# Optimization experiments

Hardware: AMD Instinct MI355X
Metric: run time of the kernel (lower is better)

## Reference

```python
import jax, jax.numpy as jnp
import numpy as np


def setup_inputs() -> dict:
    key = jax.random.key(0)
    kq, kk, kv = jax.random.split(key, 3)
    B, H, T, D = 1, 16, 4096, 64
    Q = jax.random.normal(kq, (B, H, T, D), dtype=jnp.float32)
    K = jax.random.normal(kk, (B, H, T, D), dtype=jnp.float32)
    V = jax.random.normal(kv, (B, H, T, D), dtype=jnp.float32)
    return {"Q": Q, "K": K, "V": V}


def reference(Q, K, V):
    B, H, T, D = Q.shape
    # ALiBi slopes: m_h = 2^(-8*h/H), h = 1..H (deterministic buffer)
    slopes = jnp.exp2(-8.0 * jnp.arange(1, H + 1, dtype=jnp.float32) / H)
    pos = jnp.arange(T, dtype=jnp.float32)
    dist = jnp.abs(pos[None, :] - pos[:, None])          # (T, T)
    bias = slopes[:, None, None] * dist                   # (H, T, T)
    scale = jnp.sqrt(jnp.asarray(D, dtype=Q.dtype))
    scores = jnp.einsum('bhtd,bhsd->bhts', Q, K) / scale - bias[None]
    attn = jax.nn.softmax(scores, axis=-1)
    return jnp.einsum('bhts,bhsd->bhtd', attn, V)
```

## Files before the change

kernel.cpp:

```cpp
#include <hip/hip_runtime.h>
#include <hip/hip_bf16.h>
#include <stdint.h>

typedef float f4    __attribute__((ext_vector_type(4)));
typedef float f32x4 __attribute__((ext_vector_type(4)));
typedef short s16x8 __attribute__((ext_vector_type(8)));
typedef short s16x4 __attribute__((ext_vector_type(4)));
typedef unsigned short u16;

#define T_LEN 4096
#define NHEAD 16
#define DHEAD 64
#define KVBLK 64
#define NT    (T_LEN / KVBLK)

#if __has_builtin(__builtin_amdgcn_exp2f)
#define EXP2(x) __builtin_amdgcn_exp2f(x)
#else
#define EXP2(x) exp2f(x)
#endif

#define SLOT_F 8320
#define CONV_BYTES ((size_t)16777216)
#define SLOTS_BAL  1152
#define BAL_BYTES  (CONV_BYTES + (size_t)SLOTS_BAL * SLOT_F * 4u)

__device__ __constant__ int NCARR[8] = {2,2,3,5,6,6,6,6};
__device__ __constant__ int SBARR[8] = {1088,1024,928,768,576,384,192,0};

__device__ __forceinline__ uint32_t pk2(float a, float b){
  uint32_t ua = __builtin_bit_cast(uint32_t, a) + 0x8000u;
  uint32_t ub = __builtin_bit_cast(uint32_t, b) + 0x8000u;
  return __builtin_amdgcn_perm(ub, ua, 0x07060302u);
}
__device__ __forceinline__ int swk(int r){ return (r ^ (r >> 3)) & 7; }
__device__ __forceinline__ int sw(int r){ return swk(r) << 3; }

__global__ __launch_bounds__(256)
void cvt_kv(const float* __restrict__ K, const float* __restrict__ V,
            u16* __restrict__ Kb, u16* __restrict__ VT){
  __shared__ u16 tile[64][66];
  if (blockIdx.x < 2048){
    const size_t i = ((size_t)blockIdx.x * 256 + threadIdx.x) * 8;
    f4 a = *(const f4*)(K + i);
    f4 b = *(const f4*)(K + i + 4);
    union { uint32_t w[4]; s16x8 v; } u;
    u.w[0] = pk2(a[0], a[1]); u.w[1] = pk2(a[2], a[3]);
    u.w[2] = pk2(b[0], b[1]); u.w[3] = pk2(b[2], b[3]);
    *(s16x8*)(Kb + i) = u.v;
  } else {
    const int vb = blockIdx.x - 2048;
    const int h  = vb >> 6;
    const int kt = vb & 63;
    const int t  = threadIdx.x;
    const float* Vh = V + ((size_t)h * T_LEN + kt * 64) * DHEAD;

    const int r = t >> 2, c = (t & 3) * 16;
    f4 x0 = *(const f4*)(Vh + r*64 + c);
    f4 x1 = *(const f4*)(Vh + r*64 + c + 4);
    f4 x2 = *(const f4*)(Vh + r*64 + c + 8);
    f4 x3 = *(const f4*)(Vh + r*64 + c + 12);
    uint32_t* tp = (uint32_t*)&tile[r][c];
    tp[0] = pk2(x0[0],x0[1]); tp[1] = pk2(x0[2],x0[3]);
    tp[2] = pk2(x1[0],x1[1]); tp[3] = pk2(x1[2],x1[3]);
    tp[4] = pk2(x2[0],x2[1]); tp[5] = pk2(x2[2],x2[3]);
    tp[6] = pk2(x3[0],x3[1]); tp[7] = pk2(x3[2],x3[3]);
    __syncthreads();

    const int d = t >> 2, ks = (t & 3) * 16;
    u16* op = VT + ((size_t)h * DHEAD + d) * T_LEN + kt * 64 + ks;
    union { uint32_t w[4]; s16x8 v; } o0, o1;
#pragma unroll
    for (int q = 0; q < 4; ++q)
      o0.w[q] = (uint32_t)tile[ks + 2*q][d]     | ((uint32_t)tile[ks + 2*q + 1][d] << 16);
#pragma unroll
    for (int q = 0; q < 4; ++q)
      o1.w[q] = (uint32_t)tile[ks + 8 + 2*q][d] | ((uint32_t)tile[ks + 9 + 2*q][d] << 16);
    *(s16x8*)(op)     = o0.v;
    *(s16x8*)(op + 8) = o1.v;
  }
}

__global__ __launch_bounds__(256, 2)
void alibi_attn8(const float* __restrict__ Qg,
                 const u16* __restrict__ Kb,
                 const u16* __restrict__ VTb,
                 float* __restrict__ Og,
                 float* __restrict__ part)
{
  __shared__ u16 kbuf[2][KVBLK * DHEAD];
  __shared__ u16 vbuf[2][DHEAD * KVBLK];

  int h, qt, c, n, sb;
  {
    int r = blockIdx.x;
    if (r < 768){
      h = 15 - r / 192; r %= 192; n = 6; qt = r / 6; c = r % 6; sb = (15 - h) * 192;
    } else if ((r -= 768) < 160){
      h = 11; n = 5; qt = r / 5; c = r % 5; sb = 768;
    } else if ((r -= 160) < 96){
      h = 10; n = 3; qt = r / 3; c = r % 3; sb = 928;
    } else if ((r -= 96) < 64){
      h = 9; n = 2; qt = r >> 1; c = r & 1; sb = 1024;
    } else if ((r -= 64) < 64){
      h = 8; n = 2; qt = r >> 1; c = r & 1; sb = 1088;
    } else {
      r -= 64; h = r >> 5; qt = r & 31; n = 1; c = 0; sb = 0;
    }
  }

  const int tid  = threadIdx.x;
  const int wv   = tid >> 6;
  const int lane = tid & 63;
  const int lg   = lane >> 4;
  const int ln   = lane & 15;

  const int q0   = qt * 128;
  const int qr0  = q0 + wv * 32 + ln;
  const float slope = exp2f(-0.5f * (float)(h + 1));
  const float cs = 0.125f * 1.44269504089f;
  const float bs = slope * 1.44269504089f;
  const size_t headoff = (size_t)h * T_LEN * DHEAD;

  const int Di = (int)(36.0f / bs);
  int lo = (q0 - Di) >> 6;           if (lo < 0) lo = 0;
  int hi = (q0 + 127 + Di) >> 6;     if (hi > NT - 1) hi = NT - 1;
  const int len = hi - lo + 1;
  const int start = lo + (c * len) / n;
  const int end   = lo + ((c + 1) * len) / n;

  s16x8 qf[2][2];
#pragma unroll
  for (int rg = 0; rg < 2; ++rg){
    const float* qp = Qg + headoff + (size_t)(qr0 + rg*16) * DHEAD + lg * 8;
    f4 x = *(const f4*)qp;        f4 y = *(const f4*)(qp + 4);
    f4 z = *(const f4*)(qp + 32); f4 v = *(const f4*)(qp + 36);
    union { uint32_t w_[4]; s16x8 v_; } u0, u1;
    u0.w_[0] = pk2(x[0]*cs, x[1]*cs); u0.w_[1] = pk2(x[2]*cs, x[3]*cs);
    u0.w_[2] = pk2(y[0]*cs, y[1]*cs); u0.w_[3] = pk2(y[2]*cs, y[3]*cs);
    u1.w_[0] = pk2(z[0]*cs, z[1]*cs); u1.w_[1] = pk2(z[2]*cs, z[3]*cs);
    u1.w_[2] = pk2(v[0]*cs, v[1]*cs); u1.w_[3] = pk2(v[2]*cs, v[3]*cs);
    qf[rg][0] = u0.v_; qf[rg][1] = u1.v_;
  }

  f32x4 acc[2][4];
#pragma unroll
  for (int rg = 0; rg < 2; ++rg)
#pragma unroll
    for (int dt = 0; dt < 4; ++dt) acc[rg][dt] = (f32x4)(0.0f);
  float lsum[2] = {0.0f, 0.0f};
  const float b0 = (float)qr0 - (float)(lg * 4);

  int koffs[4][2];
#pragma unroll
  for (int kt = 0; kt < 4; ++kt){
    const int key = kt*16 + ln, sz = sw(key);
    koffs[kt][0] = (((key*64      + lg*8) ^ sz)) * 2;
    koffs[kt][1] = (((key*64 + 32 + lg*8) ^ sz)) * 2;
  }
  int voffs[4][4];
#pragma unroll
  for (int dt = 0; dt < 4; ++dt){
    const int d = dt*16 + ln, sz = sw(d);
#pragma unroll
    for (int kt = 0; kt < 4; ++kt)
      voffs[dt][kt] = (((d*64 + kt*16 + lg*4) ^ sz)) * 2;
  }

  const u16* Kh = Kb  + headoff;
  const u16* Vh = VTb + headoff;
  const int sA = wv * 128 + lane;
  const int sB = sA + 64;
  const int keyA = sA >> 3, gA = (sA & 7) ^ swk(keyA);
  const int keyB = sB >> 3, gB = (sB & 7) ^ swk(keyB);
  const int kidxA = keyA * 64 + gA * 8;
  const int kidxB = keyB * 64 + gB * 8;
  const int vidxA = keyA * T_LEN + gA * 8;
  const int vidxB = keyB * T_LEN + gB * 8;
  const int dstA = sA * 16, dstB = sB * 16;

  s16x8 rkA, rkB, rvA, rvB;
  auto ldregs = [&](int t){
    const u16* kp = Kh + (size_t)t * (KVBLK * DHEAD);
    const u16* vp = Vh + (size_t)t * KVBLK;
    rkA = *(const s16x8*)(kp + kidxA);  rkB = *(const s16x8*)(kp + kidxB);
    rvA = *(const s16x8*)(vp + vidxA);  rvB = *(const s16x8*)(vp + vidxB);
  };
  auto wrregs = [&](u16* kb_, u16* vb_){
    *(s16x8*)((char*)kb_ + dstA) = rkA;  *(s16x8*)((char*)kb_ + dstB) = rkB;
    *(s16x8*)((char*)vb_ + dstA) = rvA;  *(s16x8*)((char*)vb_ + dstB) = rvB;
  };

  auto compute = [&](const u16* kb_, const u16* vb_, int kv){
    f32x4 S[2][4];
    __builtin_amdgcn_s_setprio(1);
#pragma unroll
    for (int kt = 0; kt < 4; ++kt){
      s16x8 k0 = *(const s16x8*)((const char*)kb_ + koffs[kt][0]);
      s16x8 k1 = *(const s16x8*)((const char*)kb_ + koffs[kt][1]);
      f32x4 c0 = (f32x4)(0.0f), c1 = (f32x4)(0.0f);
      c0 = __builtin_amdgcn_mfma_f32_16x16x32_bf16(k0, qf[0][0], c0, 0, 0, 0);
      c0 = __builtin_amdgcn_mfma_f32_16x16x32_bf16(k1, qf[0][1], c0, 0, 0, 0);
      c1 = __builtin_amdgcn_mfma_f32_16x16x32_bf16(k0, qf[1][0], c1, 0, 0, 0);
      c1 = __builtin_amdgcn_mfma_f32_16x16x32_bf16(k1, qf[1][1], c1, 0, 0, 0);
      S[0][kt] = c0; S[1][kt] = c1;
    }
    __builtin_amdgcn_s_setprio(0);

    s16x4 pb[2][4];
#pragma unroll
    for (int rg = 0; rg < 2; ++rg){
      const float bi = b0 + (float)(rg * 16) - (float)(kv * KVBLK);
#pragma unroll
      for (int kt = 0; kt < 4; ++kt)
#pragma unroll
        for (int r = 0; r < 4; ++r)
          S[rg][kt][r] = EXP2(fmaf(-bs, fabsf(bi - (float)(kt*16 + r)), S[rg][kt][r]));

      lsum[rg] += (((S[rg][0][0]+S[rg][0][1]) + (S[rg][0][2]+S[rg][0][3]))
                +  ((S[rg][1][0]+S[rg][1][1]) + (S[rg][1][2]+S[rg][1][3])))
                + (((S[rg][2][0]+S[rg][2][1]) + (S[rg][2][2]+S[rg][2][3]))
                +  ((S[rg][3][0]+S[rg][3][1]) + (S[rg][3][2]+S[rg][3][3])));

#pragma unroll
      for (int kt = 0; kt < 4; ++kt){
        union { uint32_t w_[2]; s16x4 v_; } u;
        u.w_[0] = pk2(S[rg][kt][0], S[rg][kt][1]);
        u.w_[1] = pk2(S[rg][kt][2], S[rg][kt][3]);
        pb[rg][kt] = u.v_;
      }
    }

    __builtin_amdgcn_s_setprio(1);
#pragma unroll
    for (int dt = 0; dt < 4; ++dt){
#pragma unroll
      for (int kt = 0; kt < 4; ++kt){
        const s16x4 vf = *(const s16x4*)((const char*)vb_ + voffs[dt][kt]);
        acc[0][dt] = __builtin_amdgcn_mfma_f32_16x16x16bf16_1k(vf, pb[0][kt], acc[0][dt], 0, 0, 0);
        acc[1][dt] = __builtin_amdgcn_mfma_f32_16x16x16bf16_1k(vf, pb[1][kt], acc[1][dt], 0, 0, 0);
      }
    }
    __builtin_amdgcn_s_setprio(0);
  };

  {
    ldregs(start);
    wrregs(kbuf[0], vbuf[0]);
    __syncthreads();

    const int hi_i = end - 1;
    int t = start;
#pragma unroll 1
    while (t + 1 < hi_i){
      ldregs(t + 1);
      compute(kbuf[0], vbuf[0], t);
      wrregs(kbuf[1], vbuf[1]);
      __syncthreads();
      ldregs(t + 2);
      compute(kbuf[1], vbuf[1], t + 1);
      wrregs(kbuf[0], vbuf[0]);
      __syncthreads();
      t += 2;
    }
    if (t < hi_i){
      ldregs(t + 1);
      compute(kbuf[0], vbuf[0], t);
      wrregs(kbuf[1], vbuf[1]);
      __syncthreads();
      compute(kbuf[1], vbuf[1], t + 1);
    } else {
      compute(kbuf[0], vbuf[0], t);
    }
  }

#pragma unroll
  for (int rg = 0; rg < 2; ++rg){
    lsum[rg] += __shfl_xor(lsum[rg], 16, 64);
    lsum[rg] += __shfl_xor(lsum[rg], 32, 64);
  }

  if (n == 1){
#pragma unroll
    for (int rg = 0; rg < 2; ++rg){
      const float inv = 1.0f / lsum[rg];
      float* op = Og + headoff + (size_t)(qr0 + rg*16) * DHEAD + lg * 4;
#pragma unroll
      for (int dt = 0; dt < 4; ++dt){
        f4 o;
        o[0] = acc[rg][dt][0] * inv; o[1] = acc[rg][dt][1] * inv;
        o[2] = acc[rg][dt][2] * inv; o[3] = acc[rg][dt][3] * inv;
        *(f4*)(op + dt*16) = o;
      }
    }
  } else {
    float* slot = part + (size_t)(sb + qt * n + c) * SLOT_F;
#pragma unroll
    for (int rg = 0; rg < 2; ++rg){
      const int row = wv * 32 + rg * 16 + ln;
      float* op = slot + row * 64 + lg * 4;
#pragma unroll
      for (int dt = 0; dt < 4; ++dt)
        *(f4*)(op + dt*16) = acc[rg][dt];
      if (lg == 0) slot[8192 + row] = lsum[rg];
    }
  }
}

__global__ __launch_bounds__(256)
void combine_k(const float* __restrict__ part, float* __restrict__ Og){
  const int h  = 8 + (blockIdx.x >> 5);
  const int qt = blockIdx.x & 31;
  const int n  = NCARR[h - 8];
  const int sb = SBARR[h - 8] + qt * n;

  const int t   = threadIdx.x;
  const int row = t >> 1;
  const int seg = (t & 1) * 32;

  f4 a[8];
#pragma unroll
  for (int i = 0; i < 8; ++i) a[i] = (f4)(0.0f);
  float l = 0.0f;
#pragma unroll 1
  for (int c = 0; c < n; ++c){
    const float* sp = part + (size_t)(sb + c) * SLOT_F;
    const float* rp = sp + row * 64 + seg;
#pragma unroll
    for (int i = 0; i < 8; ++i) a[i] += *(const f4*)(rp + i*4);
    l += sp[8192 + row];
  }
  const float inv = 1.0f / l;
  float* op = Og + (((size_t)h * T_LEN + qt * 128 + row) * DHEAD) + seg;
#pragma unroll
  for (int i = 0; i < 8; ++i){
    f4 o;
    o[0] = a[i][0]*inv; o[1] = a[i][1]*inv; o[2] = a[i][2]*inv; o[3] = a[i][3]*inv;
    *(f4*)(op + i*4) = o;
  }
}

__global__ __launch_bounds__(256, 4)
void alibi_attn4(const float* __restrict__ Qg,
                 const u16* __restrict__ Kb,
                 const u16* __restrict__ VTb,
                 float* __restrict__ Og)
{
  __shared__ u16 kbuf[2][KVBLK * DHEAD];
  __shared__ u16 vbuf[2][DHEAD * KVBLK];

  const int bid = blockIdx.x;
  const int fid = (bid & 7) * 128 + (bid >> 3);
  const int h  = fid & 15;
  const int qt = fid >> 4;

  const int tid  = threadIdx.x;
  const int wv   = tid >> 6;
  const int lane = tid & 63;
  const int lg   = lane >> 4;
  const int ln   = lane & 15;

  const int q0   = qt * 64;
  const int qrow = q0 + wv * 16 + ln;
  const float slope = exp2f(-0.5f * (float)(h + 1));
  const float cs = 0.125f * 1.44269504089f;
  const float bs = slope * 1.44269504089f;
  const size_t headoff = (size_t)h * T_LEN * DHEAD;

  const int Di = (int)(36.0f / bs);
  int lo = (q0 - Di) >> 6;           if (lo < 0) lo = 0;
  int hi = (q0 + 63 + Di) >> 6;      if (hi > NT - 1) hi = NT - 1;

  s16x8 qf0, qf1;
  {
    const float* qp = Qg + headoff + (size_t)qrow * DHEAD + lg * 8;
    f4 x = *(const f4*)qp;        f4 y = *(const f4*)(qp + 4);
    f4 z = *(const f4*)(qp + 32); f4 v = *(const f4*)(qp + 36);
    union { uint32_t w_[4]; s16x8 v_; } u0, u1;
    u0.w_[0] = pk2(x[0]*cs, x[1]*cs); u0.w_[1] = pk2(x[2]*cs, x[3]*cs);
    u0.w_[2] = pk2(y[0]*cs, y[1]*cs); u0.w_[3] = pk2(y[2]*cs, y[3]*cs);
    u1.w_[0] = pk2(z[0]*cs, z[1]*cs); u1.w_[1] = pk2(z[2]*cs, z[3]*cs);
    u1.w_[2] = pk2(v[0]*cs, v[1]*cs); u1.w_[3] = pk2(v[2]*cs, v[3]*cs);
    qf0 = u0.v_; qf1 = u1.v_;
  }

  f32x4 acc[4];
#pragma unroll
  for (int dt = 0; dt < 4; ++dt) acc[dt] = (f32x4)(0.0f);
  float lsum = 0.0f;
  const float base0 = (float)qrow - (float)(lg * 4);

  int koffs[4][2];
#pragma unroll
  for (int kt = 0; kt < 4; ++kt){
    const int key = kt*16 + ln, sz = sw(key);
    koffs[kt][0] = (((key*64      + lg*8) ^ sz)) * 2;
    koffs[kt][1] = (((key*64 + 32 + lg*8) ^ sz)) * 2;
  }
  int voffs[4][4];
#pragma unroll
  for (int dt = 0; dt < 4; ++dt){
    const int d = dt*16 + ln, sz = sw(d);
#pragma unroll
    for (int kt = 0; kt < 4; ++kt)
      voffs[dt][kt] = (((d*64 + kt*16 + lg*4) ^ sz)) * 2;
  }

  const u16* Kh = Kb  + headoff;
  const u16* Vh = VTb + headoff;
  const int sA = wv * 128 + lane;
  const int sB = sA + 64;
  const int keyA = sA >> 3, gA = (sA & 7) ^ swk(keyA);
  const int keyB = sB >> 3, gB = (sB & 7) ^ swk(keyB);
  const int kidxA = keyA * 64 + gA * 8;
  const int kidxB = keyB * 64 + gB * 8;
  const int vidxA = keyA * T_LEN + gA * 8;
  const int vidxB = keyB * T_LEN + gB * 8;
  const int dstA = sA * 16, dstB = sB * 16;

  s16x8 rkA, rkB, rvA, rvB;
  auto ldregs = [&](int t){
    const u16* kp = Kh + (size_t)t * (KVBLK * DHEAD);
    const u16* vp = Vh + (size_t)t * KVBLK;
    rkA = *(const s16x8*)(kp + kidxA);  rkB = *(const s16x8*)(kp + kidxB);
    rvA = *(const s16x8*)(vp + vidxA);  rvB = *(const s16x8*)(vp + vidxB);
  };
  auto wrregs = [&](u16* kb_, u16* vb_){
    *(s16x8*)((char*)kb_ + dstA) = rkA;  *(s16x8*)((char*)kb_ + dstB) = rkB;
    *(s16x8*)((char*)vb_ + dstA) = rvA;  *(s16x8*)((char*)vb_ + dstB) = rvB;
  };

  auto compute = [&](const u16* kb_, const u16* vb_, int kv){
    f32x4 S[4];
    __builtin_amdgcn_s_setprio(1);
#pragma unroll
    for (int kt = 0; kt < 4; ++kt){
      s16x8 k0 = *(const s16x8*)((const char*)kb_ + koffs[kt][0]);
      s16x8 k1 = *(const s16x8*)((const char*)kb_ + koffs[kt][1]);
      f32x4 cc = (f32x4)(0.0f);
      cc = __builtin_amdgcn_mfma_f32_16x16x32_bf16(k0, qf0, cc, 0, 0, 0);
      cc = __builtin_amdgcn_mfma_f32_16x16x32_bf16(k1, qf1, cc, 0, 0, 0);
      S[kt] = cc;
    }
    __builtin_amdgcn_s_setprio(0);

    const float bi = base0 - (float)(kv * KVBLK);
    float p[16];
#pragma unroll
    for (int kt = 0; kt < 4; ++kt)
#pragma unroll
      for (int r = 0; r < 4; ++r)
        p[kt*4 + r] = EXP2(fmaf(-bs, fabsf(bi - (float)(kt*16 + r)), S[kt][r]));

    lsum += (((p[0]+p[1]) + (p[2]+p[3])) + ((p[4]+p[5]) + (p[6]+p[7])))
          + (((p[8]+p[9]) + (p[10]+p[11])) + ((p[12]+p[13]) + (p[14]+p[15])));

    s16x4 pb[4];
#pragma unroll
    for (int kt = 0; kt < 4; ++kt){
      union { uint32_t w_[2]; s16x4 v_; } u;
      u.w_[0] = pk2(p[kt*4+0], p[kt*4+1]);
      u.w_[1] = pk2(p[kt*4+2], p[kt*4+3]);
      pb[kt] = u.v_;
    }

    __builtin_amdgcn_s_setprio(1);
#pragma unroll
    for (int dt = 0; dt < 4; ++dt){
#pragma unroll
      for (int kt = 0; kt < 4; ++kt){
        const s16x4 vf = *(const s16x4*)((const char*)vb_ + voffs[dt][kt]);
        acc[dt] = __builtin_amdgcn_mfma_f32_16x16x16bf16_1k(vf, pb[kt], acc[dt], 0, 0, 0);
      }
    }
    __builtin_amdgcn_s_setprio(0);
  };

  ldregs(lo);
  wrregs(kbuf[0], vbuf[0]);
  __syncthreads();

  int t = lo;
#pragma unroll 1
  while (t + 1 < hi){
    ldregs(t + 1);
    compute(kbuf[0], vbuf[0], t);
    wrregs(kbuf[1], vbuf[1]);
    __syncthreads();
    ldregs(t + 2);
    compute(kbuf[1], vbuf[1], t + 1);
    wrregs(kbuf[0], vbuf[0]);
    __syncthreads();
    t += 2;
  }
  if (t < hi){
    ldregs(t + 1);
    compute(kbuf[0], vbuf[0], t);
    wrregs(kbuf[1], vbuf[1]);
    __syncthreads();
    compute(kbuf[1], vbuf[1], t + 1);
  } else {
    compute(kbuf[0], vbuf[0], t);
  }

  lsum += __shfl_xor(lsum, 16, 64);
  lsum += __shfl_xor(lsum, 32, 64);
  const float inv = 1.0f / lsum;
  float* op = Og + headoff + (size_t)qrow * DHEAD + lg * 4;
#pragma unroll
  for (int dt = 0; dt < 4; ++dt){
    f4 o;
    o[0] = acc[dt][0] * inv; o[1] = acc[dt][1] * inv;
    o[2] = acc[dt][2] * inv; o[3] = acc[dt][3] * inv;
    *(f4*)(op + dt*16) = o;
  }
}

__global__ __launch_bounds__(256, 2)
void alibi_attn_fb(const float* __restrict__ Qg,
                   const float* __restrict__ Kg,
                   const float* __restrict__ Vg,
                   float* __restrict__ Og)
{
  __shared__ u16 kbuf[2][KVBLK * DHEAD];
  __shared__ u16 vbuf[2][DHEAD * KVBLK];

  const int bid = blockIdx.x;
  const int fid = (bid & 7) * 64 + (bid >> 3);
  const int h  = fid >> 5;
  const int qt = fid & 31;

  const int tid  = threadIdx.x;
  const int wave = tid >> 6;
  const int lane = tid & 63;
  const int lg   = lane >> 4;
  const int ln   = lane & 15;

  const int qb = qt * 128 + wave * 32;
  const float slope = exp2f(-0.5f * (float)(h + 1));
  const float cs = 0.125f * 1.44269504089f;
  const float bs = slope * 1.44269504089f;
  const size_t headoff = (size_t)h * T_LEN * DHEAD;

  s16x8 qf[2][2];
#pragma unroll
  for (int rg = 0; rg < 2; ++rg)
#pragma unroll
    for (int dh = 0; dh < 2; ++dh){
      const float* qp = Qg + headoff + (size_t)(qb + rg*16 + ln) * DHEAD + dh*32 + lg*8;
      f4 x = *(const f4*)qp;
      f4 y = *(const f4*)(qp + 4);
      union { uint32_t w[4]; s16x8 v; } u;
      u.w[0] = pk2(x[0]*cs, x[1]*cs);
      u.w[1] = pk2(x[2]*cs, x[3]*cs);
      u.w[2] = pk2(y[0]*cs, y[1]*cs);
      u.w[3] = pk2(y[2]*cs, y[3]*cs);
      qf[rg][dh] = u.v;
    }

  f32x4 acc[2][4];
#pragma unroll
  for (int rg = 0; rg < 2; ++rg)
#pragma unroll
    for (int dt = 0; dt < 4; ++dt) acc[rg][dt] = (f32x4)(0.0f);
  float mreg[2] = {-1e30f, -1e30f};
  float lreg[2] = {0.0f, 0.0f};
  const float qposf[2] = {(float)(qb + ln), (float)(qb + 16 + ln)};
  const float koffb = (float)(lg * 4);

  f4 st4[8];
  const int vk0  = (tid >> 2) * 2;
  const int vseg = (tid & 3) * 16;
  const int krow = (tid - 128) >> 1;
  const int kseg = ((tid - 128) & 1) * 32;
  const float* Vb = Vg + headoff;
  const float* Kb_ = Kg + headoff;

  auto stage_load = [&](int kv){
    const int kb = kv * KVBLK;
    if (tid < 128){
      const float* vp = Vb + (size_t)(kb + vk0) * DHEAD + vseg;
      st4[0] = *(const f4*)(vp);      st4[1] = *(const f4*)(vp + 4);
      st4[2] = *(const f4*)(vp + 8);  st4[3] = *(const f4*)(vp + 12);
      st4[4] = *(const f4*)(vp + 64); st4[5] = *(const f4*)(vp + 68);
      st4[6] = *(const f4*)(vp + 72); st4[7] = *(const f4*)(vp + 76);
    } else {
      const float* kp = Kb_ + (size_t)(kb + krow) * DHEAD + kseg;
#pragma unroll
      for (int j = 0; j < 8; ++j) st4[j] = *(const f4*)(kp + j*4);
    }
  };
  auto stage_store = [&](int b){
    if (tid < 128){
#pragma unroll
      for (int i = 0; i < 16; ++i){
        const int d = vseg + i;
        uint32_t pr = pk2(st4[i>>2][i&3], st4[4 + (i>>2)][i&3]);
        *(uint32_t*)&vbuf[b][(d*64 + vk0) ^ sw(d)] = pr;
      }
    } else {
#pragma unroll
      for (int i = 0; i < 4; ++i){
        union { uint32_t w[4]; s16x8 v; } u;
        u.w[0] = pk2(st4[i*2][0],   st4[i*2][1]);
        u.w[1] = pk2(st4[i*2][2],   st4[i*2][3]);
        u.w[2] = pk2(st4[i*2+1][0], st4[i*2+1][1]);
        u.w[3] = pk2(st4[i*2+1][2], st4[i*2+1][3]);
        *(s16x8*)&kbuf[b][(krow*64 + kseg + i*8) ^ sw(krow)] = u.v;
      }
    }
  };

  stage_load(0);
  stage_store(0);
  __syncthreads();
  int cur = 0;

#pragma unroll 1
  for (int kv = 0; kv < NT; ++kv){
    if (kv + 1 < NT) stage_load(kv + 1);

    const float kbf = (float)(kv * KVBLK);
    const u16* kb_ = kbuf[cur];
    const u16* vb_ = vbuf[cur];

    s16x8 kf[4][2];
#pragma unroll
    for (int kt = 0; kt < 4; ++kt){
      const int key = kt*16 + ln;
      const int sz  = sw(key);
      kf[kt][0] = *(const s16x8*)&kb_[(key*64 +      lg*8) ^ sz];
      kf[kt][1] = *(const s16x8*)&kb_[(key*64 + 32 + lg*8) ^ sz];
    }
    f32x4 S[2][4];
#pragma unroll
    for (int rg = 0; rg < 2; ++rg)
#pragma unroll
      for (int kt = 0; kt < 4; ++kt){
        f32x4 c = (f32x4)(0.0f);
        c = __builtin_amdgcn_mfma_f32_16x16x32_bf16(kf[kt][0], qf[rg][0], c, 0, 0, 0);
        c = __builtin_amdgcn_mfma_f32_16x16x32_bf16(kf[kt][1], qf[rg][1], c, 0, 0, 0);
        S[rg][kt] = c;
      }

    s16x4 pb[2][4];
#pragma unroll
    for (int rg = 0; rg < 2; ++rg){
      const float base = qposf[rg] - kbf - koffb;
#pragma unroll
      for (int kt = 0; kt < 4; ++kt)
#pragma unroll
        for (int r = 0; r < 4; ++r)
          S[rg][kt][r] = fmaf(-bs, fabsf(base - (float)(kt*16 + r)), S[rg][kt][r]);

      float a0 = fmaxf(fmaxf(S[rg][0][0], S[rg][0][1]), fmaxf(S[rg][0][2], S[rg][0][3]));
      float a1 = fmaxf(fmaxf(S[rg][1][0], S[rg][1][1]), fmaxf(S[rg][1][2], S[rg][1][3]));
      float a2 = fmaxf(fmaxf(S[rg][2][0], S[rg][2][1]), fmaxf(S[rg][2][2], S[rg][2][3]));
      float a3 = fmaxf(fmaxf(S[rg][3][0], S[rg][3][1]), fmaxf(S[rg][3][2], S[rg][3][3]));
      float mx = fmaxf(fmaxf(a0, a1), fmaxf(a2, a3));
      mx = fmaxf(mx, __shfl_xor(mx, 16, 64));
      mx = fmaxf(mx, __shfl_xor(mx, 32, 64));

      const float mo = mreg[rg];
      const float mn = fmaxf(mo, mx);
      const float scl = EXP2(mo - mn);
      mreg[rg] = mn;

      float p[16];
#pragma unroll
      for (int kt = 0; kt < 4; ++kt)
#pragma unroll
        for (int r = 0; r < 4; ++r)
          p[kt*4 + r] = EXP2(S[rg][kt][r] - mn);

      float s0 = (p[0]+p[1]) + (p[2]+p[3]);
      float s1 = (p[4]+p[5]) + (p[6]+p[7]);
      float s2 = (p[8]+p[9]) + (p[10]+p[11]);
      float s3 = (p[12]+p[13]) + (p[14]+p[15]);
      float sum = (s0+s1) + (s2+s3);
      sum += __shfl_xor(sum, 16, 64);
      sum += __shfl_xor(sum, 32, 64);
      lreg[rg] = lreg[rg] * scl + sum;

#pragma unroll
      for (int dt = 0; dt < 4; ++dt) acc[rg][dt] *= scl;

#pragma unroll
      for (int kt = 0; kt < 4; ++kt){
        union { uint32_t w[2]; s16x4 v; } u;
        u.w[0] = pk2(p[kt*4+0], p[kt*4+1]);
        u.w[1] = pk2(p[kt*4+2], p[kt*4+3]);
        pb[rg][kt] = u.v;
      }
    }

#pragma unroll
    for (int dt = 0; dt < 4; ++dt){
      const int d  = dt*16 + ln;
      const int sz = sw(d);
#pragma unroll
      for (int kt = 0; kt < 4; ++kt){
        const s16x4 vf = *(const s16x4*)&vb_[(d*64 + kt*16 + lg*4) ^ sz];
        acc[0][dt] = __builtin_amdgcn_mfma_f32_16x16x16bf16_1k(vf, pb[0][kt], acc[0][dt], 0, 0, 0);
        acc[1][dt] = __builtin_amdgcn_mfma_f32_16x16x16bf16_1k(vf, pb[1][kt], acc[1][dt], 0, 0, 0);
      }
    }

    if (kv + 1 < NT){
      stage_store(cur ^ 1);
      __syncthreads();
      cur ^= 1;
    }
  }

#pragma unroll
  for (int rg = 0; rg < 2; ++rg){
    const float inv = 1.0f / lreg[rg];
    float* op = Og + headoff + (size_t)(qb + rg*16 + ln) * DHEAD + lg*4;
#pragma unroll
    for (int dt = 0; dt < 4; ++dt){
      f4 o;
      o[0] = acc[rg][dt][0] * inv;
      o[1] = acc[rg][dt][1] * inv;
      o[2] = acc[rg][dt][2] * inv;
      o[3] = acc[rg][dt][3] * inv;
      *(f4*)(op + dt*16) = o;
    }
  }
}

extern "C" void kernel_launch(void* const* d_in, const int* in_sizes, int n_in,
                              void* d_out, int out_size, void* d_ws, size_t ws_size,
                              hipStream_t stream)
{
  const float* Q = (const float*)d_in[0];
  const float* K = (const float*)d_in[1];
  const float* V = (const float*)d_in[2];
  float* O = (float*)d_out;

  if (ws_size >= BAL_BYTES){
    u16* Kb = (u16*)d_ws;
    u16* VT = Kb + (size_t)NHEAD * T_LEN * DHEAD;
    float* part = (float*)((char*)d_ws + CONV_BYTES);
    hipLaunchKernelGGL(cvt_kv, dim3(3072), dim3(256), 0, stream, K, V, Kb, VT);
    hipLaunchKernelGGL(alibi_attn8, dim3(1408), dim3(256), 0, stream, Q, Kb, VT, O, part);
    hipLaunchKernelGGL(combine_k, dim3(256), dim3(256), 0, stream, part, O);
  } else if (ws_size >= CONV_BYTES){
    u16* Kb = (u16*)d_ws;
    u16* VT = Kb + (size_t)NHEAD * T_LEN * DHEAD;
    hipLaunchKernelGGL(cvt_kv, dim3(3072), dim3(256), 0, stream, K, V, Kb, VT);
    hipLaunchKernelGGL(alibi_attn4, dim3(1024), dim3(256), 0, stream, Q, Kb, VT, O);
  } else {
    hipLaunchKernelGGL(alibi_attn_fb, dim3(512), dim3(256), 0, stream, Q, K, V, O);
  }
}
```

Measured before the change: 86.62 us.

## Triple-buffer K/V tiles in LDS with two-deep register prefetch

Replaces the double-buffered K/V pipeline with a three-slot LDS ring and two sets of staging registers. Global loads are issued two tiles ahead and LDS writes one tile ahead, so only one barrier is needed per tile instead of syncing around each write. This aims to hide global memory latency and reduce barrier stalls. The cost is more LDS per block and more staging registers, which may reduce occupancy or cause spills.

```diff
diff --git a/kernel.cpp b/kernel.cpp
--- a/kernel.cpp
+++ b/kernel.cpp
@@ -82,14 +82,14 @@
 }
 
 __global__ __launch_bounds__(256, 2)
-void alibi_attn8(const float* __restrict__ Qg,
+void alibi_attn9(const float* __restrict__ Qg,
                  const u16* __restrict__ Kb,
                  const u16* __restrict__ VTb,
                  float* __restrict__ Og,
                  float* __restrict__ part)
 {
-  __shared__ u16 kbuf[2][KVBLK * DHEAD];
-  __shared__ u16 vbuf[2][DHEAD * KVBLK];
+  __shared__ u16 kbuf[3][KVBLK * DHEAD];
+  __shared__ u16 vbuf[3][DHEAD * KVBLK];
 
   int h, qt, c, n, sb;
   {
@@ -149,7 +149,7 @@
 #pragma unroll
     for (int dt = 0; dt < 4; ++dt) acc[rg][dt] = (f32x4)(0.0f);
   float lsum[2] = {0.0f, 0.0f};
-  const float b0 = (float)qr0 - (float)(lg * 4);
+  const float b0f = (float)qr0 - (float)(lg * 4);
 
   int koffs[4][2];
 #pragma unroll
@@ -179,16 +179,27 @@
   const int vidxB = keyB * T_LEN + gB * 8;
   const int dstA = sA * 16, dstB = sB * 16;
 
-  s16x8 rkA, rkB, rvA, rvB;
-  auto ldregs = [&](int t){
+  s16x8 Ak0, Ak1, Av0, Av1, Bk0, Bk1, Bv0, Bv1;
+  auto ldset = [&](int t){
     const u16* kp = Kh + (size_t)t * (KVBLK * DHEAD);
     const u16* vp = Vh + (size_t)t * KVBLK;
-    rkA = *(const s16x8*)(kp + kidxA);  rkB = *(const s16x8*)(kp + kidxB);
-    rvA = *(const s16x8*)(vp + vidxA);  rvB = *(const s16x8*)(vp + vidxB);
+    if ((t & 1) == 0){
+      Ak0 = *(const s16x8*)(kp + kidxA);  Ak1 = *(const s16x8*)(kp + kidxB);
+      Av0 = *(const s16x8*)(vp + vidxA);  Av1 = *(const s16x8*)(vp + vidxB);
+    } else {
+      Bk0 = *(const s16x8*)(kp + kidxA);  Bk1 = *(const s16x8*)(kp + kidxB);
+      Bv0 = *(const s16x8*)(vp + vidxA);  Bv1 = *(const s16x8*)(vp + vidxB);
+    }
   };
-  auto wrregs = [&](u16* kb_, u16* vb_){
-    *(s16x8*)((char*)kb_ + dstA) = rkA;  *(s16x8*)((char*)kb_ + dstB) = rkB;
-    *(s16x8*)((char*)vb_ + dstA) = rvA;  *(s16x8*)((char*)vb_ + dstB) = rvB;
+  auto wrset = [&](int t, int b){
+    u16* kb_ = kbuf[b];  u16* vb_ = vbuf[b];
+    if ((t & 1) == 0){
+      *(s16x8*)((char*)kb_ + dstA) = Ak0;  *(s16x8*)((char*)kb_ + dstB) = Ak1;
+      *(s16x8*)((char*)vb_ + dstA) = Av0;  *(s16x8*)((char*)vb_ + dstB) = Av1;
+    } else {
+      *(s16x8*)((char*)kb_ + dstA) = Bk0;  *(s16x8*)((char*)kb_ + dstB) = Bk1;
+      *(s16x8*)((char*)vb_ + dstA) = Bv0;  *(s16x8*)((char*)vb_ + dstB) = Bv1;
+    }
   };
 
   auto compute = [&](const u16* kb_, const u16* vb_, int kv){
@@ -210,7 +221,7 @@
     s16x4 pb[2][4];
 #pragma unroll
     for (int rg = 0; rg < 2; ++rg){
-      const float bi = b0 + (float)(rg * 16) - (float)(kv * KVBLK);
+      const float bi = b0f + (float)(rg * 16) - (float)(kv * KVBLK);
 #pragma unroll
       for (int kt = 0; kt < 4; ++kt)
 #pragma unroll
@@ -245,33 +256,22 @@
   };
 
   {
-    ldregs(start);
-    wrregs(kbuf[0], vbuf[0]);
-    __syncthreads();
-
-    const int hi_i = end - 1;
-    int t = start;
+    ldset(start);
+    if (start + 1 < end) ldset(start + 1);
+    wrset(start, start % 3);
+    asm volatile("s_waitcnt lgkmcnt(0)" ::: "memory");
+    __builtin_amdgcn_s_barrier();
+  }
+
+  int bc = start % 3, bn = (start + 1) % 3, bf_ = (start + 2) % 3;
 #pragma unroll 1
-    while (t + 1 < hi_i){
-      ldregs(t + 1);
-      compute(kbuf[0], vbuf[0], t);
-      wrregs(kbuf[1], vbuf[1]);
-      __syncthreads();
-      ldregs(t + 2);
-      compute(kbuf[1], vbuf[1], t + 1);
-      wrregs(kbuf[0], vbuf[0]);
-      __syncthreads();
-      t += 2;
-    }
-    if (t < hi_i){
-      ldregs(t + 1);
-      compute(kbuf[0], vbuf[0], t);
-      wrregs(kbuf[1], vbuf[1]);
-      __syncthreads();
-      compute(kbuf[1], vbuf[1], t + 1);
-    } else {
-      compute(kbuf[0], vbuf[0], t);
-    }
+  for (int t = start; t < end; ++t){
+    if (t + 2 < end) ldset(t + 2);
+    if (t + 1 < end) wrset(t + 1, bn);
+    compute(kbuf[bc], vbuf[bc], t);
+    asm volatile("s_waitcnt lgkmcnt(0)" ::: "memory");
+    __builtin_amdgcn_s_barrier();
+    const int tmp = bc; bc = bn; bn = bf_; bf_ = tmp;
   }
 
 #pragma unroll
@@ -743,7 +743,7 @@
     u16* VT = Kb + (size_t)NHEAD * T_LEN * DHEAD;
     float* part = (float*)((char*)d_ws + CONV_BYTES);
     hipLaunchKernelGGL(cvt_kv, dim3(3072), dim3(256), 0, stream, K, V, Kb, VT);
-    hipLaunchKernelGGL(alibi_attn8, dim3(1408), dim3(256), 0, stream, Q, Kb, VT, O, part);
+    hipLaunchKernelGGL(alibi_attn9, dim3(1408), dim3(256), 0, stream, Q, Kb, VT, O, part);
     hipLaunchKernelGGL(combine_k, dim3(256), dim3(256), 0, stream, part, O);
   } else if (ws_size >= CONV_BYTES){
     u16* Kb = (u16*)d_ws;
```

Measured after the change: 102.6 us. 1.18x slower.
